# Optimization experiments

Hardware: AMD Instinct MI355X
Metric: run time of the kernel (lower is better)

Reference implementation:

```python
import jax, jax.numpy as jnp
import numpy as np

B, T, C, H = 8, 1024, 512, 8


def setup_inputs() -> dict:
    key = jax.random.key(0)
    k1, k2, k3, k4 = jax.random.split(key, 4)
    x = jax.random.normal(k1, (B, T, C), jnp.float32)
    q = jax.random.normal(k2, (B, T, C), jnp.float32)
    W_kv = jax.random.normal(k3, (C, 2 * C), jnp.float32) * 0.02
    W_proj = jax.random.normal(k4, (C, C), jnp.float32) * 0.02
    return {"x": x, "q": q, "W_kv": W_kv, "W_proj": W_proj}


def reference(x, q, W_kv, W_proj):
    B, T, C = x.shape
    H = 8
    D = C // H
    T2 = T // 2
    # kv projection (nn.Linear, no bias)
    kv = x @ W_kv                      # [B,T,2C]
    k, v = kv[..., :C], kv[..., C:]
    # 7 batch-dim rolls of the first half, then reinterpret [7,B,T2,C] -> [B,7*T2,C]
    # (exactly what torch.stack(...).view(B,-1,C) does on the contiguous buffer)
    sk = jnp.stack([jnp.roll(k[:, :T2], i, axis=0) for i in range(7)]).reshape(B, -1, C)
    sv = jnp.stack([jnp.roll(v[:, :T2], i, axis=0) for i in range(7)]).reshape(B, -1, C)
    k = jnp.concatenate((sk, k), axis=1)   # [B, S, C], S = 7*T2 + T
    v = jnp.concatenate((sv, v), axis=1)
    qh = q.reshape(B, T, H, D).transpose(0, 2, 1, 3)    # [B,H,T,D]
    kh = k.reshape(B, -1, H, D).transpose(0, 2, 1, 3)   # [B,H,S,D]
    vh = v.reshape(B, -1, H, D).transpose(0, 2, 1, 3)   # [B,H,S,D]
    scale = 1.0 / jnp.sqrt(jnp.float32(D))
    # NOTE: the torch module passes attn_mask=None to SDPA, so attention is unmasked
    scores = jnp.einsum('bhld,bhsd->bhls', qh, kh) * scale
    attn = jax.nn.softmax(scores, axis=-1)
    y = jnp.einsum('bhls,bhsd->bhld', attn, vh)
    y = y.transpose(0, 2, 1, 3).reshape(B, T, C)
    return y @ W_proj
```

## Files before the change

kernel.cpp:

```cpp
#include <hip/hip_runtime.h>

typedef __bf16 bf16;
typedef bf16 bf16x8 __attribute__((ext_vector_type(8)));
typedef bf16 bf16x4 __attribute__((ext_vector_type(4)));
typedef float f32x4 __attribute__((ext_vector_type(4)));
typedef float f32x16 __attribute__((ext_vector_type(16)));
typedef unsigned int u32;

#define DEV_INLINE __device__ __forceinline__

DEV_INLINE f32x4 mfma16(bf16x8 a, bf16x8 b, f32x4 c) {
    return __builtin_amdgcn_mfma_f32_16x16x32_bf16(a, b, c, 0, 0, 0);
}
DEV_INLINE f32x16 mfma32(bf16x8 a, bf16x8 b, f32x16 c) {
    return __builtin_amdgcn_mfma_f32_32x32x16_bf16(a, b, c, 0, 0, 0);
}

#define GLD16(gp, lp) __builtin_amdgcn_global_load_lds( \
    (const __attribute__((address_space(1))) void*)(gp), \
    (__attribute__((address_space(3))) void*)(lp), 16, 0, 0)

__global__ void transpose_cast_kernel(const float* __restrict__ in, bf16* __restrict__ out,
                                      int K, int N) {
    int idx = blockIdx.x * blockDim.x + threadIdx.x;
    if (idx < K * N) {
        int n = idx / K, k = idx - n * K;
        out[idx] = (bf16)in[k * N + n];
    }
}

__launch_bounds__(256, 2)
__global__ void gemm_kv_kernel(const float* __restrict__ A,
                               const bf16* __restrict__ Bt,
                               bf16* __restrict__ Kout,
                               bf16* __restrict__ Vt)
{
    __shared__ bf16 As[128][32];
    __shared__ bf16 Bs[128][32];
    const int bm = blockIdx.x, bn = blockIdx.y;
    const int tid = threadIdx.x;
    const int lane = tid & 63, w = tid >> 6;
    const int wm = (w >> 1) * 64, wn = (w & 1) * 64;
    const int lr = lane & 15, kg = lane >> 4;

    const f32x4 fz = {0.f, 0.f, 0.f, 0.f};
    f32x4 acc[4][4];
    for (int i = 0; i < 4; ++i)
        for (int j = 0; j < 4; ++j) acc[i][j] = fz;

    const int srow = tid >> 2, sc4 = tid & 3;

    for (int k0 = 0; k0 < 512; k0 += 32) {
        __syncthreads();
        for (int rr = 0; rr < 2; ++rr) {
            int row = srow + rr * 64;
            const float* ap = A + (size_t)(bm * 128 + row) * 512 + k0 + (sc4 << 3);
            f32x4 a0 = *reinterpret_cast<const f32x4*>(ap);
            f32x4 a1 = *reinterpret_cast<const f32x4*>(ap + 4);
            bf16x8 av;
            for (int j = 0; j < 4; ++j) { av[j] = (bf16)a0[j]; av[4 + j] = (bf16)a1[j]; }
            *reinterpret_cast<bf16x8*>(&As[row][(sc4 ^ (row & 3)) << 3]) = av;
            *reinterpret_cast<bf16x8*>(&Bs[row][(sc4 ^ (row & 3)) << 3]) =
                *reinterpret_cast<const bf16x8*>(Bt + (size_t)(bn * 128 + row) * 512 + k0 + (sc4 << 3));
        }
        __syncthreads();
        bf16x8 af[4], bfr[4];
        for (int mi = 0; mi < 4; ++mi) {
            int row = wm + mi * 16 + lr;
            af[mi] = *reinterpret_cast<const bf16x8*>(&As[row][(kg ^ (row & 3)) << 3]);
        }
        for (int ni = 0; ni < 4; ++ni) {
            int row = wn + ni * 16 + lr;
            bfr[ni] = *reinterpret_cast<const bf16x8*>(&Bs[row][(kg ^ (row & 3)) << 3]);
        }
        for (int mi = 0; mi < 4; ++mi)
            for (int ni = 0; ni < 4; ++ni)
                acc[mi][ni] = mfma16(af[mi], bfr[ni], acc[mi][ni]);
    }

    for (int mi = 0; mi < 4; ++mi) {
        int mbase = bm * 128 + wm + mi * 16 + kg * 4;
        for (int ni = 0; ni < 4; ++ni) {
            int col = bn * 128 + wn + ni * 16 + lr;
            if (col < 512) {
                for (int r = 0; r < 4; ++r)
                    Kout[(size_t)(mbase + r) * 512 + col] = (bf16)acc[mi][ni][r];
            } else {
                int c = col - 512, h = c >> 6, d = c & 63;
                int b = mbase >> 10, t = mbase & 1023;
                int tp = (t & ~12) | ((t & 4) << 1) | ((t & 8) >> 1);
                bf16x4 pk;
                for (int r = 0; r < 4; ++r) pk[r] = (bf16)acc[mi][ni][r];
                *reinterpret_cast<bf16x4*>(Vt + (size_t)((b * 8 + h) * 64 + d) * 1024 + tp) = pk;
            }
        }
    }
}

__launch_bounds__(256, 2)
__global__ void gemm_proj_kernel(const bf16* __restrict__ Op,
                                 const float* __restrict__ Lp,
                                 const bf16* __restrict__ Bt,
                                 float* __restrict__ out)
{
    __shared__ bf16 As[128][32];
    __shared__ bf16 Bs[128][32];
    const int bm = blockIdx.x, bn = blockIdx.y;
    const int tid = threadIdx.x;
    const int lane = tid & 63, w = tid >> 6;
    const int wm = (w >> 1) * 64, wn = (w & 1) * 64;
    const int lr = lane & 15, kg = lane >> 4;

    const f32x4 fz = {0.f, 0.f, 0.f, 0.f};
    f32x4 acc[4][4];
    for (int i = 0; i < 4; ++i)
        for (int j = 0; j < 4; ++j) acc[i][j] = fz;

    const int srow = tid >> 2, sc4 = tid & 3;

    for (int k0 = 0; k0 < 512; k0 += 32) {
        __syncthreads();
        for (int rr = 0; rr < 2; ++rr) {
            int row = srow + rr * 64;
            int grow = bm * 128 + row;
            int kc = k0 + (sc4 << 3);
            int hh = kc >> 6;
            float l = Lp[hh * 8192 + grow] + Lp[65536 + hh * 8192 + grow];
            float inv = 1.0f / l;
            size_t off = (size_t)grow * 512 + kc;
            bf16x8 a = *reinterpret_cast<const bf16x8*>(Op + off);
            bf16x8 c = *reinterpret_cast<const bf16x8*>(Op + 4194304 + off);
            bf16x8 av;
            for (int j = 0; j < 8; ++j)
                av[j] = (bf16)(((float)a[j] + (float)c[j]) * inv);
            *reinterpret_cast<bf16x8*>(&As[row][(sc4 ^ (row & 3)) << 3]) = av;
            *reinterpret_cast<bf16x8*>(&Bs[row][(sc4 ^ (row & 3)) << 3]) =
                *reinterpret_cast<const bf16x8*>(Bt + (size_t)(bn * 128 + row) * 512 + k0 + (sc4 << 3));
        }
        __syncthreads();
        bf16x8 af[4], bfr[4];
        for (int mi = 0; mi < 4; ++mi) {
            int row = wm + mi * 16 + lr;
            af[mi] = *reinterpret_cast<const bf16x8*>(&As[row][(kg ^ (row & 3)) << 3]);
        }
        for (int ni = 0; ni < 4; ++ni) {
            int row = wn + ni * 16 + lr;
            bfr[ni] = *reinterpret_cast<const bf16x8*>(&Bs[row][(kg ^ (row & 3)) << 3]);
        }
        for (int mi = 0; mi < 4; ++mi)
            for (int ni = 0; ni < 4; ++ni)
                acc[mi][ni] = mfma16(af[mi], bfr[ni], acc[mi][ni]);
    }

    for (int mi = 0; mi < 4; ++mi) {
        int mbase = bm * 128 + wm + mi * 16 + kg * 4;
        for (int ni = 0; ni < 4; ++ni) {
            int col = bn * 128 + wn + ni * 16 + lr;
            for (int r = 0; r < 4; ++r)
                out[(size_t)(mbase + r) * 512 + col] = acc[mi][ni][r];
        }
    }
}

__launch_bounds__(512, 2)
__global__ void attn_kernel(const float* __restrict__ Qr,
                            const bf16* __restrict__ Kb,
                            const bf16* __restrict__ Vt,
                            bf16* __restrict__ Op,
                            float* __restrict__ Lp)
{
    __shared__ bf16 sK[2][64][64];
    __shared__ bf16 sV[2][64][64];

    const int raw = blockIdx.x;
    const int h = raw & 7;
    const int shalf = (raw >> 3) & 1;
    const int qseg = (raw >> 4) & 3;
    const int b = raw >> 6;
    const int tid = threadIdx.x, lane = tid & 63, w = tid >> 6;
    const int lq = lane & 31, hi = lane >> 5;
    const int qrow = b * 1024 + qseg * 256 + w * 32 + lq;
    const int sbase = shalf * 2304;

    const float QSC = 0.18033688011112306f;
    bf16x8 qf[4];
#pragma unroll
    for (int ds = 0; ds < 4; ++ds) {
        const float* qp = Qr + (size_t)qrow * 512 + h * 64 + ds * 16 + hi * 8;
        f32x4 q0 = *reinterpret_cast<const f32x4*>(qp);
        f32x4 q1 = *reinterpret_cast<const f32x4*>(qp + 4);
#pragma unroll
        for (int j = 0; j < 4; ++j) {
            qf[ds][j]     = (bf16)(q0[j] * QSC);
            qf[ds][4 + j] = (bf16)(q1[j] * QSC);
        }
    }

    const f32x16 Z16 = {0,0,0,0,0,0,0,0,0,0,0,0,0,0,0,0};
    f32x16 O0 = Z16, O1 = Z16, lv = Z16;

    const bf16* Kf = &sK[0][0][0];
    const bf16* Vf = &sV[0][0][0];
    int koffE[4], voffE[4];
#pragma unroll
    for (int ds = 0; ds < 4; ++ds) {
        koffE[ds] = lq * 64 + (((ds * 2 + hi) ^ (lq & 7)) * 8);
        voffE[ds] = lq * 64 + (((ds * 2 + hi) ^ (lq & 7)) * 8);
    }

    const int srow = w * 8 + (lane >> 3);
    const int schunk = (lane & 7) ^ (srow & 7);
    const size_t koff = (size_t)srow * 512 + schunk * 8;
    const size_t voff = (size_t)srow * 1024 + schunk * 8;

    auto kv_base = [&](int t, const bf16*& kp, const bf16*& vp) {
        int gs = sbase + t * 64;
        int jj = gs >> 9, tin = gs & 511;
        if (jj < 7) {
            int m7 = 7 * b + jj;
            int src_b = ((m7 & 7) - (m7 >> 3)) & 7;
            kp = Kb + (size_t)(src_b * 1024 + tin) * 512 + h * 64;
            vp = Vt + (size_t)((src_b * 8 + h) * 64) * 1024 + tin;
        } else {
            int tpos = (jj - 7) * 512 + tin;
            kp = Kb + (size_t)(b * 1024 + tpos) * 512 + h * 64;
            vp = Vt + (size_t)((b * 8 + h) * 64) * 1024 + tpos;
        }
    };

    auto stage = [&](int buf, int t) {
        const bf16 *kp, *vp;
        kv_base(t, kp, vp);
        GLD16(kp + koff, &sK[buf][w * 8][0]);
        GLD16(vp + voff, &sV[buf][w * 8][0]);
    };

    auto computeTile = [&](int cb) {
        const int kb = cb * 4096;
        f32x16 s0, s1;
        __builtin_amdgcn_s_setprio(1);
        {
            bf16x8 k0 = *reinterpret_cast<const bf16x8*>(Kf + kb + koffE[0]);
            bf16x8 k1 = *reinterpret_cast<const bf16x8*>(Kf + kb + 2048 + koffE[0]);
            s0 = mfma32(k0, qf[0], Z16);
            s1 = mfma32(k1, qf[0], Z16);
        }
#pragma unroll
        for (int ds = 1; ds < 4; ++ds) {
            bf16x8 k0 = *reinterpret_cast<const bf16x8*>(Kf + kb + koffE[ds]);
            bf16x8 k1 = *reinterpret_cast<const bf16x8*>(Kf + kb + 2048 + koffE[ds]);
            s0 = mfma32(k0, qf[ds], s0);
            s1 = mfma32(k1, qf[ds], s1);
        }
        __builtin_amdgcn_s_setprio(0);

#pragma unroll
        for (int i = 0; i < 16; ++i) {
            float p0 = __builtin_amdgcn_exp2f(s0[i]); s0[i] = p0;
            float p1 = __builtin_amdgcn_exp2f(s1[i]); s1[i] = p1;
            lv[i] += p0 + p1;
        }

        __builtin_amdgcn_s_setprio(1);
#pragma unroll
        for (int ssub = 0; ssub < 4; ++ssub) {
            bf16x8 pf;
#pragma unroll
            for (int i = 0; i < 8; ++i) {
                float pv = (ssub < 2) ? ((ssub & 1) ? s0[8 + i] : s0[i])
                                      : ((ssub & 1) ? s1[8 + i] : s1[i]);
                pf[i] = (bf16)pv;
            }
            bf16x8 a0 = *reinterpret_cast<const bf16x8*>(Vf + kb + voffE[ssub]);
            bf16x8 a1 = *reinterpret_cast<const bf16x8*>(Vf + kb + 2048 + voffE[ssub]);
            O0 = mfma32(a0, pf, O0);
            O1 = mfma32(a1, pf, O1);
        }
        __builtin_amdgcn_s_setprio(0);
    };

    stage(0, 0);

    for (int t = 0; t < 36; t += 2) {
        __syncthreads();
        stage(1, t + 1);
        computeTile(0);
        __syncthreads();
        if (t + 2 < 36) stage(0, t + 2);
        computeTile(1);
    }

    float lrun = 0.f;
#pragma unroll
    for (int i = 0; i < 16; ++i) lrun += lv[i];
    lrun += __shfl_xor(lrun, 32);
    if (hi == 0) Lp[shalf * 65536 + h * 8192 + qrow] = lrun;

    bf16* Od = Op + (size_t)shalf * 4194304;
#pragma unroll
    for (int dh = 0; dh < 2; ++dh) {
#pragma unroll
        for (int q4 = 0; q4 < 4; ++q4) {
            bf16x4 pk;
#pragma unroll
            for (int i = 0; i < 4; ++i)
                pk[i] = (bf16)(dh ? O1[q4 * 4 + i] : O0[q4 * 4 + i]);
            *reinterpret_cast<bf16x4*>(
                Od + (size_t)qrow * 512 + h * 64 + dh * 32 + q4 * 8 + hi * 4) = pk;
        }
    }
}

extern "C" void kernel_launch(void* const* d_in, const int* in_sizes, int n_in,
                              void* d_out, int out_size, void* d_ws, size_t ws_size,
                              hipStream_t stream) {
    const float* x   = (const float*)d_in[0];
    const float* q   = (const float*)d_in[1];
    const float* Wkv = (const float*)d_in[2];
    const float* Wp  = (const float*)d_in[3];
    float* out = (float*)d_out;

    char* ws = (char*)d_ws;
    bf16*  Kb   = (bf16*)(ws);
    bf16*  Vt   = (bf16*)(ws + 8388608);
    bf16*  Opar = (bf16*)(ws + 16777216);
    bf16*  Wkvt = (bf16*)(ws + 41943040);
    bf16*  Wpt  = (bf16*)(ws + 42991616);
    float* Lp   = (float*)(ws + 43515904);

    transpose_cast_kernel<<<(512 * 1024) / 256, 256, 0, stream>>>(Wkv, Wkvt, 512, 1024);
    transpose_cast_kernel<<<(512 * 512) / 256, 256, 0, stream>>>(Wp, Wpt, 512, 512);
    gemm_kv_kernel<<<dim3(64, 8), 256, 0, stream>>>(x, Wkvt, Kb, Vt);
    attn_kernel<<<512, 512, 0, stream>>>(q, Kb, Vt, Opar, Lp);
    gemm_proj_kernel<<<dim3(64, 4), 256, 0, stream>>>(Opar, Lp, Wpt, out);
}
```

Baseline: 126.2 us.

## Pre-cast x to bf16 and double-buffer KV GEMM with direct global-to-LDS loads

A new cast kernel converts x to bf16 in workspace before the GEMM. The KV projection GEMM then loads both operands with global_load_lds into double-buffered shared tiles, overlapping the next tile's load with the current MFMA step. The projection GEMM also moves its weight tile loads to global_load_lds. The trade-off is an extra kernel launch plus one extra read and write of x, and more LDS per block.

```diff
diff --git a/kernel.cpp b/kernel.cpp
--- a/kernel.cpp
+++ b/kernel.cpp
@@ -20,6 +20,16 @@
     (const __attribute__((address_space(1))) void*)(gp), \
     (__attribute__((address_space(3))) void*)(lp), 16, 0, 0)
 
+__global__ void cast_kernel(const float* __restrict__ in, bf16* __restrict__ out, int n4) {
+    int i = blockIdx.x * blockDim.x + threadIdx.x;
+    if (i < n4) {
+        f32x4 v = reinterpret_cast<const f32x4*>(in)[i];
+        bf16x4 o;
+        o[0] = (bf16)v[0]; o[1] = (bf16)v[1]; o[2] = (bf16)v[2]; o[3] = (bf16)v[3];
+        reinterpret_cast<bf16x4*>(out)[i] = o;
+    }
+}
+
 __global__ void transpose_cast_kernel(const float* __restrict__ in, bf16* __restrict__ out,
                                       int K, int N) {
     int idx = blockIdx.x * blockDim.x + threadIdx.x;
@@ -30,13 +40,13 @@
 }
 
 __launch_bounds__(256, 2)
-__global__ void gemm_kv_kernel(const float* __restrict__ A,
+__global__ void gemm_kv_kernel(const bf16* __restrict__ A,
                                const bf16* __restrict__ Bt,
                                bf16* __restrict__ Kout,
                                bf16* __restrict__ Vt)
 {
-    __shared__ bf16 As[128][32];
-    __shared__ bf16 Bs[128][32];
+    __shared__ bf16 As[2][128][32];
+    __shared__ bf16 Bs[2][128][32];
     const int bm = blockIdx.x, bn = blockIdx.y;
     const int tid = threadIdx.x;
     const int lane = tid & 63, w = tid >> 6;
@@ -48,34 +58,46 @@
     for (int i = 0; i < 4; ++i)
         for (int j = 0; j < 4; ++j) acc[i][j] = fz;
 
-    const int srow = tid >> 2, sc4 = tid & 3;
-
-    for (int k0 = 0; k0 < 512; k0 += 32) {
-        __syncthreads();
-        for (int rr = 0; rr < 2; ++rr) {
-            int row = srow + rr * 64;
-            const float* ap = A + (size_t)(bm * 128 + row) * 512 + k0 + (sc4 << 3);
-            f32x4 a0 = *reinterpret_cast<const f32x4*>(ap);
-            f32x4 a1 = *reinterpret_cast<const f32x4*>(ap + 4);
-            bf16x8 av;
-            for (int j = 0; j < 4; ++j) { av[j] = (bf16)a0[j]; av[4 + j] = (bf16)a1[j]; }
-            *reinterpret_cast<bf16x8*>(&As[row][(sc4 ^ (row & 3)) << 3]) = av;
-            *reinterpret_cast<bf16x8*>(&Bs[row][(sc4 ^ (row & 3)) << 3]) =
-                *reinterpret_cast<const bf16x8*>(Bt + (size_t)(bn * 128 + row) * 512 + k0 + (sc4 << 3));
-        }
-        __syncthreads();
+    const int rrow = lane >> 2;
+    const int chnk = lane & 3;
+
+    auto stage = [&](int buf, int k0) {
+#pragma unroll
+        for (int j = 0; j < 2; ++j) {
+            int row = w * 32 + j * 16 + rrow;
+            int sc = ((chnk ^ (row & 3)) << 3);
+            GLD16(A  + (size_t)(bm * 128 + row) * 512 + k0 + sc, &As[buf][w * 32 + j * 16][0]);
+            GLD16(Bt + (size_t)(bn * 128 + row) * 512 + k0 + sc, &Bs[buf][w * 32 + j * 16][0]);
+        }
+    };
+
+    auto computeStep = [&](int buf) {
         bf16x8 af[4], bfr[4];
+#pragma unroll
         for (int mi = 0; mi < 4; ++mi) {
             int row = wm + mi * 16 + lr;
-            af[mi] = *reinterpret_cast<const bf16x8*>(&As[row][(kg ^ (row & 3)) << 3]);
-        }
+            af[mi] = *reinterpret_cast<const bf16x8*>(&As[buf][row][(kg ^ (row & 3)) << 3]);
+        }
+#pragma unroll
         for (int ni = 0; ni < 4; ++ni) {
             int row = wn + ni * 16 + lr;
-            bfr[ni] = *reinterpret_cast<const bf16x8*>(&Bs[row][(kg ^ (row & 3)) << 3]);
-        }
+            bfr[ni] = *reinterpret_cast<const bf16x8*>(&Bs[buf][row][(kg ^ (row & 3)) << 3]);
+        }
+#pragma unroll
         for (int mi = 0; mi < 4; ++mi)
+#pragma unroll
             for (int ni = 0; ni < 4; ++ni)
                 acc[mi][ni] = mfma16(af[mi], bfr[ni], acc[mi][ni]);
+    };
+
+    stage(0, 0);
+    for (int kk = 0; kk < 512; kk += 64) {
+        __syncthreads();
+        stage(1, kk + 32);
+        computeStep(0);
+        __syncthreads();
+        if (kk + 64 < 512) stage(0, kk + 64);
+        computeStep(1);
     }
 
     for (int mi = 0; mi < 4; ++mi) {
@@ -117,9 +139,16 @@
         for (int j = 0; j < 4; ++j) acc[i][j] = fz;
 
     const int srow = tid >> 2, sc4 = tid & 3;
+    const int rrow = lane >> 2, chnk = lane & 3;
 
     for (int k0 = 0; k0 < 512; k0 += 32) {
         __syncthreads();
+#pragma unroll
+        for (int j = 0; j < 2; ++j) {
+            int rowB = w * 32 + j * 16 + rrow;
+            int scB = ((chnk ^ (rowB & 3)) << 3);
+            GLD16(Bt + (size_t)(bn * 128 + rowB) * 512 + k0 + scB, &Bs[w * 32 + j * 16][0]);
+        }
         for (int rr = 0; rr < 2; ++rr) {
             int row = srow + rr * 64;
             int grow = bm * 128 + row;
@@ -134,8 +163,6 @@
             for (int j = 0; j < 8; ++j)
                 av[j] = (bf16)(((float)a[j] + (float)c[j]) * inv);
             *reinterpret_cast<bf16x8*>(&As[row][(sc4 ^ (row & 3)) << 3]) = av;
-            *reinterpret_cast<bf16x8*>(&Bs[row][(sc4 ^ (row & 3)) << 3]) =
-                *reinterpret_cast<const bf16x8*>(Bt + (size_t)(bn * 128 + row) * 512 + k0 + (sc4 << 3));
         }
         __syncthreads();
         bf16x8 af[4], bfr[4];
@@ -324,13 +351,16 @@
     bf16*  Kb   = (bf16*)(ws);
     bf16*  Vt   = (bf16*)(ws + 8388608);
     bf16*  Opar = (bf16*)(ws + 16777216);
+    bf16*  xb   = (bf16*)(ws + 33554432);
     bf16*  Wkvt = (bf16*)(ws + 41943040);
     bf16*  Wpt  = (bf16*)(ws + 42991616);
     float* Lp   = (float*)(ws + 43515904);
 
+    const int n4 = 8192 * 512 / 4;
+    cast_kernel<<<n4 / 256, 256, 0, stream>>>(x, xb, n4);
     transpose_cast_kernel<<<(512 * 1024) / 256, 256, 0, stream>>>(Wkv, Wkvt, 512, 1024);
     transpose_cast_kernel<<<(512 * 512) / 256, 256, 0, stream>>>(Wp, Wpt, 512, 512);
-    gemm_kv_kernel<<<dim3(64, 8), 256, 0, stream>>>(x, Wkvt, Kb, Vt);
+    gemm_kv_kernel<<<dim3(64, 8), 256, 0, stream>>>(xb, Wkvt, Kb, Vt);
     attn_kernel<<<512, 512, 0, stream>>>(q, Kb, Vt, Opar, Lp);
     gemm_proj_kernel<<<dim3(64, 4), 256, 0, stream>>>(Opar, Lp, Wpt, out);
 }
```

Result: slower. 131.1 us (+3.9%).
